# Performance work log

Hardware: AMD Instinct MI355X
Metric: run time of the kernel (lower is better)

Reference implementation:

```python
import jax, jax.numpy as jnp
import numpy as np

B = 65536
A_CH, S_CH, D_CH = 64, 256, 256
IN_CH = A_CH + S_CH + D_CH   # 576
MID = 32
OUT_CH = 4 * S_CH            # 1024
R_IN = IN_CH + S_CH          # 832

def _xavier(key, fan_in, fan_out):
    lim = np.sqrt(6.0 / (fan_in + fan_out)).astype(np.float32)
    return jax.random.uniform(key, (fan_in, fan_out), jnp.float32, -lim, lim)

def setup_inputs() -> dict:
    key = jax.random.key(0)
    ks = jax.random.split(key, 8)
    return {
        "prev_h": jax.random.normal(ks[0], (B, S_CH), jnp.float32),
        "prev_c": jax.random.normal(ks[1], (B, S_CH), jnp.float32),
        "action": jax.random.normal(ks[2], (B, A_CH), jnp.float32),
        "dynamics": jax.random.normal(ks[3], (B, D_CH), jnp.float32),
        "W1": _xavier(ks[4], IN_CH, MID),
        "b1": jnp.zeros((MID,), jnp.float32),
        "W2": _xavier(ks[5], MID, OUT_CH),
        "b2": jnp.zeros((OUT_CH,), jnp.float32),
        "Wr": _xavier(ks[6], R_IN, 1),
        "br": jnp.zeros((1,), jnp.float32),
    }

def reference(prev_h, prev_c, action, dynamics, W1, b1, W2, b2, Wr, br):
    # concat order matches torch: [dynamics, action, prev_h] -> [B, 576]
    x = jnp.concatenate([dynamics, action, prev_h], axis=1)
    h1 = jnp.tanh(x @ W1 + b1)            # fc1: tanh activation, [B, 32]
    g = h1 @ W2 + b2                       # fc2: no activation, [B, 4*S]
    act_i, act_f, hat_c, act_o = jnp.split(g, 4, axis=1)
    act_i = jax.nn.sigmoid(act_i)
    act_f = jax.nn.sigmoid(act_f)
    hat_c = jnp.tanh(hat_c)
    act_o = jax.nn.sigmoid(act_o)
    next_c = act_f * prev_c + act_i * hat_c
    next_h = act_o * jnp.tanh(next_c)
    xr = jnp.concatenate([x, next_h], axis=1)  # [B, 832]
    reward = jnp.tanh(xr @ Wr + br)            # [B, 1]
    return next_h, next_c, reward
```

## Files before the change

kernel.cpp:

```cpp
#include <hip/hip_runtime.h>
#include <hip/hip_bf16.h>

typedef float f32x4 __attribute__((ext_vector_type(4)));
typedef short bf16x8 __attribute__((ext_vector_type(8)));
typedef float float4v __attribute__((ext_vector_type(4)));

#define H1_STRIDE 40
#define W1T_K 576
#define W2T_OFF (48 * 576)

__device__ __forceinline__ short f2bf(float f) {
  __bf16 b = (__bf16)f;
  return __builtin_bit_cast(short, b);
}
__device__ __forceinline__ float fast_sigmoid(float x) {
  return __builtin_amdgcn_rcpf(1.f + __expf(-x));
}
__device__ __forceinline__ float fast_tanh(float x) {
  float e = __expf(2.f * x);
  return 1.f - 2.f * __builtin_amdgcn_rcpf(e + 1.f);
}

__global__ __launch_bounds__(256) void prep_weights(
    const float* __restrict__ W1, const float* __restrict__ W2,
    const float* __restrict__ Wr, short* __restrict__ ws)
{
  int i = blockIdx.x * 256 + threadIdx.x;
  if (i < 48 * 576) {
    int n = i / 576;
    int k = i - n * 576;
    float v = 0.f;
    if (n < 32) v = W1[k * 32 + n];
    else if (n == 32) v = Wr[k];
    ws[i] = f2bf(v);
  } else {
    int j = i - 48 * 576;
    if (j < 32 * 1024) {
      int n = j >> 5;
      int k = j & 31;
      ws[W2T_OFF + j] = f2bf(W2[k * 1024 + n]);
    }
  }
}

__global__ __launch_bounds__(256, 4) void fclstm_main(
    const float* __restrict__ prev_h, const float* __restrict__ prev_c,
    const float* __restrict__ action, const float* __restrict__ dynamics,
    const float* __restrict__ b1, const float* __restrict__ b2,
    const float* __restrict__ Wr, const float* __restrict__ br,
    const short* __restrict__ wsw,
    float* __restrict__ out_h, float* __restrict__ out_c, float* __restrict__ out_r)
{
  __shared__ short h1T[64 * H1_STRIDE];

  const int t  = threadIdx.x;
  const int r0 = blockIdx.x * 64;

  const int wid  = t >> 6;
  const int lane = t & 63;
  const int lg   = lane >> 4;
  const int ln   = lane & 15;
  const int m0   = wid << 4;
  const int rowb = r0 + m0 + 4 * lg;

  float pcA[32];
  #pragma unroll
  for (int q = 0; q < 8; ++q) {
    #pragma unroll
    for (int r = 0; r < 4; ++r)
      pcA[q * 4 + r] = prev_c[(size_t)(rowb + r) * 256 + q * 16 + ln];
  }

  f32x4 acc0 = {0.f,0.f,0.f,0.f};
  f32x4 acc1 = {0.f,0.f,0.f,0.f};
  f32x4 acc2 = {0.f,0.f,0.f,0.f};

  const int rowA = r0 + m0 + ln;
  const int kb   = 8 * lg;
  const float* dynp = dynamics + rowA * 256 + kb;
  const float* actp = action   + rowA * 64  + kb;
  const float* hp   = prev_h   + rowA * 256 + kb;
  const short* w1f  = wsw + ln * W1T_K + kb;

  auto ldfrag = [&](const float* p) -> bf16x8 {
    float4v v0 = *(const float4v*)(p);
    float4v v1 = *(const float4v*)(p + 4);
    bf16x8 a;
    a[0] = f2bf(v0.x); a[1] = f2bf(v0.y); a[2] = f2bf(v0.z); a[3] = f2bf(v0.w);
    a[4] = f2bf(v1.x); a[5] = f2bf(v1.y); a[6] = f2bf(v1.z); a[7] = f2bf(v1.w);
    return a;
  };

  #pragma unroll
  for (int j = 0; j < 18; ++j) {
    const float* src;
    if (j < 8)       src = dynp + 32 * j;
    else if (j < 10) src = actp + 32 * j - 256;
    else             src = hp   + 32 * j - 320;
    bf16x8 a  = ldfrag(src);
    bf16x8 bA = *(const bf16x8*)(w1f + 32 * j);
    bf16x8 bB = *(const bf16x8*)(w1f + 16 * W1T_K + 32 * j);
    bf16x8 bC = *(const bf16x8*)(w1f + 32 * W1T_K + 32 * j);
    acc0 = __builtin_amdgcn_mfma_f32_16x16x32_bf16(a, bA, acc0, 0, 0, 0);
    acc1 = __builtin_amdgcn_mfma_f32_16x16x32_bf16(a, bB, acc1, 0, 0, 0);
    acc2 = __builtin_amdgcn_mfma_f32_16x16x32_bf16(a, bC, acc2, 0, 0, 0);
  }

  {
    float bc0 = b1[ln], bc1 = b1[16 + ln];
    #pragma unroll
    for (int r = 0; r < 4; ++r) {
      int row = m0 + 4 * lg + r;
      h1T[row * H1_STRIDE + ln]      = f2bf(fast_tanh(acc0[r] + bc0));
      h1T[row * H1_STRIDE + 16 + ln] = f2bf(fast_tanh(acc1[r] + bc1));
    }
  }
  asm volatile("s_waitcnt lgkmcnt(0)" ::: "memory");
  __builtin_amdgcn_sched_barrier(0);
  bf16x8 af2 = *(const bf16x8*)&h1T[(m0 + ln) * H1_STRIDE + 8 * lg];

  float pcB[32];
  #pragma unroll
  for (int q = 0; q < 8; ++q) {
    #pragma unroll
    for (int r = 0; r < 4; ++r)
      pcB[q * 4 + r] = prev_c[(size_t)(rowb + r) * 256 + (q + 8) * 16 + ln];
  }

  float racc[4] = {0.f, 0.f, 0.f, 0.f};
  const float br0 = br[0];
  const short* w2t = wsw + W2T_OFF;

  auto fc2_tile = [&](int nt, float pc0, float pc1, float pc2, float pc3) {
    const int nc_ = nt * 16 + ln;
    const short* bb = w2t + nc_ * 32 + 8 * lg;
    bf16x8 bi  = *(const bf16x8*)(bb);
    bf16x8 bf_ = *(const bf16x8*)(bb + 256 * 32);
    bf16x8 bc_ = *(const bf16x8*)(bb + 512 * 32);
    bf16x8 bo  = *(const bf16x8*)(bb + 768 * 32);
    f32x4 gi = {0.f,0.f,0.f,0.f}, gf = {0.f,0.f,0.f,0.f};
    f32x4 gc = {0.f,0.f,0.f,0.f}, go = {0.f,0.f,0.f,0.f};
    gi = __builtin_amdgcn_mfma_f32_16x16x32_bf16(af2, bi,  gi, 0, 0, 0);
    gf = __builtin_amdgcn_mfma_f32_16x16x32_bf16(af2, bf_, gf, 0, 0, 0);
    gc = __builtin_amdgcn_mfma_f32_16x16x32_bf16(af2, bc_, gc, 0, 0, 0);
    go = __builtin_amdgcn_mfma_f32_16x16x32_bf16(af2, bo,  go, 0, 0, 0);
    float b2i = b2[nc_], b2f = b2[256 + nc_], b2c = b2[512 + nc_], b2o = b2[768 + nc_];
    float wrv = Wr[576 + nc_];
    float pc_[4] = {pc0, pc1, pc2, pc3};
    #pragma unroll
    for (int r = 0; r < 4; ++r) {
      int row = rowb + r;
      float iv  = fast_sigmoid(gi[r] + b2i);
      float fv  = fast_sigmoid(gf[r] + b2f);
      float cv  = fast_tanh(gc[r] + b2c);
      float ov  = fast_sigmoid(go[r] + b2o);
      float ncv = fv * pc_[r] + iv * cv;
      float nhv = ov * fast_tanh(ncv);
      __builtin_nontemporal_store(nhv, &out_h[(size_t)row * 256 + nc_]);
      __builtin_nontemporal_store(ncv, &out_c[(size_t)row * 256 + nc_]);
      racc[r] += nhv * wrv;
    }
  };

  #pragma unroll
  for (int q = 0; q < 8; ++q)
    fc2_tile(q, pcA[q * 4 + 0], pcA[q * 4 + 1], pcA[q * 4 + 2], pcA[q * 4 + 3]);
  #pragma unroll
  for (int q = 0; q < 8; ++q)
    fc2_tile(q + 8, pcB[q * 4 + 0], pcB[q * 4 + 1], pcB[q * 4 + 2], pcB[q * 4 + 3]);

  #pragma unroll
  for (int off = 1; off < 16; off <<= 1) {
    #pragma unroll
    for (int r = 0; r < 4; ++r) racc[r] += __shfl_xor(racc[r], off, 64);
  }
  if (ln == 0) {
    #pragma unroll
    for (int r = 0; r < 4; ++r) {
      float s = acc2[r] + racc[r] + br0;
      __builtin_nontemporal_store(fast_tanh(s), &out_r[rowb + r]);
    }
  }
}

extern "C" void kernel_launch(void* const* d_in, const int* in_sizes, int n_in,
                              void* d_out, int out_size, void* d_ws, size_t ws_size,
                              hipStream_t stream) {
  const float* prev_h   = (const float*)d_in[0];
  const float* prev_c   = (const float*)d_in[1];
  const float* action   = (const float*)d_in[2];
  const float* dynamics = (const float*)d_in[3];
  const float* W1 = (const float*)d_in[4];
  const float* b1 = (const float*)d_in[5];
  const float* W2 = (const float*)d_in[6];
  const float* b2 = (const float*)d_in[7];
  const float* Wr = (const float*)d_in[8];
  const float* br = (const float*)d_in[9];
  short* wsw = (short*)d_ws;

  float* out_h = (float*)d_out;
  float* out_c = out_h + (size_t)65536 * 256;
  float* out_r = out_c + (size_t)65536 * 256;

  prep_weights<<<236, 256, 0, stream>>>(W1, W2, Wr, wsw);
  fclstm_main<<<1024, 256, 0, stream>>>(prev_h, prev_c, action, dynamics,
                                        b1, b2, Wr, br, wsw, out_h, out_c, out_r);
}
```

Before: 86.66 us.

## Transpose MFMA operands for row-per-lane layout and prefetch fc1 input loads

Swaps the MFMA A/B operands so each lane owns one batch row and four consecutive output columns. prev_c loads, bias loads and out_h/out_c stores become float4 vectors, and the reward reduction shrinks to two cross-group shuffles. It also adds a 6-deep software prefetch ring for the fc1 activation loads and moves the prev_c loads to mid-loop and post-loop positions. The aim is fewer scalar global memory transactions and better latency hiding, at the cost of more live registers.

```diff
diff --git a/kernel.cpp b/kernel.cpp
--- a/kernel.cpp
+++ b/kernel.cpp
@@ -8,10 +8,14 @@
 #define H1_STRIDE 40
 #define W1T_K 576
 #define W2T_OFF (48 * 576)
+#define PF 6
 
 __device__ __forceinline__ short f2bf(float f) {
   __bf16 b = (__bf16)f;
   return __builtin_bit_cast(short, b);
+}
+__device__ __forceinline__ uint pack2(float a, float b) {
+  return (uint)(unsigned short)f2bf(a) | ((uint)(unsigned short)f2bf(b) << 16);
 }
 __device__ __forceinline__ float fast_sigmoid(float x) {
   return __builtin_amdgcn_rcpf(1.f + __expf(-x));
@@ -61,125 +65,130 @@
   const int lg   = lane >> 4;
   const int ln   = lane & 15;
   const int m0   = wid << 4;
-  const int rowb = r0 + m0 + 4 * lg;
-
-  float pcA[32];
-  #pragma unroll
-  for (int q = 0; q < 8; ++q) {
-    #pragma unroll
-    for (int r = 0; r < 4; ++r)
-      pcA[q * 4 + r] = prev_c[(size_t)(rowb + r) * 256 + q * 16 + ln];
-  }
-
-  f32x4 acc0 = {0.f,0.f,0.f,0.f};
-  f32x4 acc1 = {0.f,0.f,0.f,0.f};
-  f32x4 acc2 = {0.f,0.f,0.f,0.f};
-
   const int rowA = r0 + m0 + ln;
+
   const int kb   = 8 * lg;
   const float* dynp = dynamics + rowA * 256 + kb;
   const float* actp = action   + rowA * 64  + kb;
   const float* hp   = prev_h   + rowA * 256 + kb;
   const short* w1f  = wsw + ln * W1T_K + kb;
-
-  auto ldfrag = [&](const float* p) -> bf16x8 {
-    float4v v0 = *(const float4v*)(p);
-    float4v v1 = *(const float4v*)(p + 4);
+  const float* pcp  = prev_c + (size_t)rowA * 256 + 4 * lg;
+
+  auto asrc = [&](int j) -> const float* {
+    return (j < 8) ? (dynp + 32 * j)
+         : (j < 10) ? (actp + 32 * j - 256)
+                    : (hp + 32 * j - 320);
+  };
+
+  f32x4 acc0 = {0.f,0.f,0.f,0.f};
+  f32x4 acc1 = {0.f,0.f,0.f,0.f};
+  f32x4 acc2 = {0.f,0.f,0.f,0.f};
+
+  float4v abuf[PF][2];
+  #pragma unroll
+  for (int j = 0; j < PF; ++j) {
+    const float* p = asrc(j);
+    abuf[j][0] = *(const float4v*)p;
+    abuf[j][1] = *(const float4v*)(p + 4);
+  }
+
+  float4v pcA[8], pcB[8];
+
+  #pragma unroll
+  for (int j = 0; j < 18; ++j) {
+    const int s = j % PF;
     bf16x8 a;
-    a[0] = f2bf(v0.x); a[1] = f2bf(v0.y); a[2] = f2bf(v0.z); a[3] = f2bf(v0.w);
-    a[4] = f2bf(v1.x); a[5] = f2bf(v1.y); a[6] = f2bf(v1.z); a[7] = f2bf(v1.w);
-    return a;
-  };
-
-  #pragma unroll
-  for (int j = 0; j < 18; ++j) {
-    const float* src;
-    if (j < 8)       src = dynp + 32 * j;
-    else if (j < 10) src = actp + 32 * j - 256;
-    else             src = hp   + 32 * j - 320;
-    bf16x8 a  = ldfrag(src);
+    {
+      float4v v0 = abuf[s][0], v1 = abuf[s][1];
+      a[0] = f2bf(v0.x); a[1] = f2bf(v0.y); a[2] = f2bf(v0.z); a[3] = f2bf(v0.w);
+      a[4] = f2bf(v1.x); a[5] = f2bf(v1.y); a[6] = f2bf(v1.z); a[7] = f2bf(v1.w);
+    }
+    if (j + PF < 18) {
+      const float* p = asrc(j + PF);
+      abuf[s][0] = *(const float4v*)p;
+      abuf[s][1] = *(const float4v*)(p + 4);
+    }
+    if (j == 8) {
+      #pragma unroll
+      for (int q = 0; q < 8; ++q) pcA[q] = *(const float4v*)(pcp + q * 16);
+    }
     bf16x8 bA = *(const bf16x8*)(w1f + 32 * j);
     bf16x8 bB = *(const bf16x8*)(w1f + 16 * W1T_K + 32 * j);
     bf16x8 bC = *(const bf16x8*)(w1f + 32 * W1T_K + 32 * j);
-    acc0 = __builtin_amdgcn_mfma_f32_16x16x32_bf16(a, bA, acc0, 0, 0, 0);
-    acc1 = __builtin_amdgcn_mfma_f32_16x16x32_bf16(a, bB, acc1, 0, 0, 0);
-    acc2 = __builtin_amdgcn_mfma_f32_16x16x32_bf16(a, bC, acc2, 0, 0, 0);
-  }
+    acc0 = __builtin_amdgcn_mfma_f32_16x16x32_bf16(bA, a, acc0, 0, 0, 0);
+    acc1 = __builtin_amdgcn_mfma_f32_16x16x32_bf16(bB, a, acc1, 0, 0, 0);
+    acc2 = __builtin_amdgcn_mfma_f32_16x16x32_bf16(bC, a, acc2, 0, 0, 0);
+  }
+
+  #pragma unroll
+  for (int q = 0; q < 8; ++q) pcB[q] = *(const float4v*)(pcp + 128 + q * 16);
 
   {
-    float bc0 = b1[ln], bc1 = b1[16 + ln];
+    float4v b1lo = *(const float4v*)&b1[4 * lg];
+    float4v b1hi = *(const float4v*)&b1[16 + 4 * lg];
+    uint2 wlo, whi;
+    wlo.x = pack2(fast_tanh(acc0[0] + b1lo.x), fast_tanh(acc0[1] + b1lo.y));
+    wlo.y = pack2(fast_tanh(acc0[2] + b1lo.z), fast_tanh(acc0[3] + b1lo.w));
+    whi.x = pack2(fast_tanh(acc1[0] + b1hi.x), fast_tanh(acc1[1] + b1hi.y));
+    whi.y = pack2(fast_tanh(acc1[2] + b1hi.z), fast_tanh(acc1[3] + b1hi.w));
+    short* hrow = &h1T[(m0 + ln) * H1_STRIDE];
+    *(uint2*)(hrow + 4 * lg)      = wlo;
+    *(uint2*)(hrow + 16 + 4 * lg) = whi;
+  }
+  asm volatile("s_waitcnt lgkmcnt(0)" ::: "memory");
+  __builtin_amdgcn_sched_barrier(0);
+  bf16x8 af2 = *(const bf16x8*)(&h1T[(m0 + ln) * H1_STRIDE] + 8 * lg);
+
+  float racc = 0.f;
+  const float br0 = br[0];
+  const short* w2t = wsw + W2T_OFF;
+  const size_t orow = (size_t)rowA * 256;
+
+  auto fc2_tile = [&](int nt, float4v pc) {
+    const int c4 = nt * 16 + 4 * lg;
+    const short* aw = w2t + (nt * 16 + ln) * 32 + 8 * lg;
+    bf16x8 wi = *(const bf16x8*)(aw);
+    bf16x8 wf = *(const bf16x8*)(aw + 256 * 32);
+    bf16x8 wc = *(const bf16x8*)(aw + 512 * 32);
+    bf16x8 wo = *(const bf16x8*)(aw + 768 * 32);
+    f32x4 gi = {0.f,0.f,0.f,0.f}, gf = {0.f,0.f,0.f,0.f};
+    f32x4 gc = {0.f,0.f,0.f,0.f}, go = {0.f,0.f,0.f,0.f};
+    gi = __builtin_amdgcn_mfma_f32_16x16x32_bf16(wi, af2, gi, 0, 0, 0);
+    gf = __builtin_amdgcn_mfma_f32_16x16x32_bf16(wf, af2, gf, 0, 0, 0);
+    gc = __builtin_amdgcn_mfma_f32_16x16x32_bf16(wc, af2, gc, 0, 0, 0);
+    go = __builtin_amdgcn_mfma_f32_16x16x32_bf16(wo, af2, go, 0, 0, 0);
+    float4v b2i = *(const float4v*)&b2[c4];
+    float4v b2f = *(const float4v*)&b2[256 + c4];
+    float4v b2c = *(const float4v*)&b2[512 + c4];
+    float4v b2o = *(const float4v*)&b2[768 + c4];
+    float4v wrv = *(const float4v*)&Wr[576 + c4];
+    float4v nh, nc2;
     #pragma unroll
     for (int r = 0; r < 4; ++r) {
-      int row = m0 + 4 * lg + r;
-      h1T[row * H1_STRIDE + ln]      = f2bf(fast_tanh(acc0[r] + bc0));
-      h1T[row * H1_STRIDE + 16 + ln] = f2bf(fast_tanh(acc1[r] + bc1));
-    }
-  }
-  asm volatile("s_waitcnt lgkmcnt(0)" ::: "memory");
-  __builtin_amdgcn_sched_barrier(0);
-  bf16x8 af2 = *(const bf16x8*)&h1T[(m0 + ln) * H1_STRIDE + 8 * lg];
-
-  float pcB[32];
-  #pragma unroll
-  for (int q = 0; q < 8; ++q) {
-    #pragma unroll
-    for (int r = 0; r < 4; ++r)
-      pcB[q * 4 + r] = prev_c[(size_t)(rowb + r) * 256 + (q + 8) * 16 + ln];
-  }
-
-  float racc[4] = {0.f, 0.f, 0.f, 0.f};
-  const float br0 = br[0];
-  const short* w2t = wsw + W2T_OFF;
-
-  auto fc2_tile = [&](int nt, float pc0, float pc1, float pc2, float pc3) {
-    const int nc_ = nt * 16 + ln;
-    const short* bb = w2t + nc_ * 32 + 8 * lg;
-    bf16x8 bi  = *(const bf16x8*)(bb);
-    bf16x8 bf_ = *(const bf16x8*)(bb + 256 * 32);
-    bf16x8 bc_ = *(const bf16x8*)(bb + 512 * 32);
-    bf16x8 bo  = *(const bf16x8*)(bb + 768 * 32);
-    f32x4 gi = {0.f,0.f,0.f,0.f}, gf = {0.f,0.f,0.f,0.f};
-    f32x4 gc = {0.f,0.f,0.f,0.f}, go = {0.f,0.f,0.f,0.f};
-    gi = __builtin_amdgcn_mfma_f32_16x16x32_bf16(af2, bi,  gi, 0, 0, 0);
-    gf = __builtin_amdgcn_mfma_f32_16x16x32_bf16(af2, bf_, gf, 0, 0, 0);
-    gc = __builtin_amdgcn_mfma_f32_16x16x32_bf16(af2, bc_, gc, 0, 0, 0);
-    go = __builtin_amdgcn_mfma_f32_16x16x32_bf16(af2, bo,  go, 0, 0, 0);
-    float b2i = b2[nc_], b2f = b2[256 + nc_], b2c = b2[512 + nc_], b2o = b2[768 + nc_];
-    float wrv = Wr[576 + nc_];
-    float pc_[4] = {pc0, pc1, pc2, pc3};
-    #pragma unroll
-    for (int r = 0; r < 4; ++r) {
-      int row = rowb + r;
-      float iv  = fast_sigmoid(gi[r] + b2i);
-      float fv  = fast_sigmoid(gf[r] + b2f);
-      float cv  = fast_tanh(gc[r] + b2c);
-      float ov  = fast_sigmoid(go[r] + b2o);
-      float ncv = fv * pc_[r] + iv * cv;
+      float iv  = fast_sigmoid(gi[r] + b2i[r]);
+      float fv  = fast_sigmoid(gf[r] + b2f[r]);
+      float cv  = fast_tanh(gc[r] + b2c[r]);
+      float ov  = fast_sigmoid(go[r] + b2o[r]);
+      float ncv = fv * pc[r] + iv * cv;
       float nhv = ov * fast_tanh(ncv);
-      __builtin_nontemporal_store(nhv, &out_h[(size_t)row * 256 + nc_]);
-      __builtin_nontemporal_store(ncv, &out_c[(size_t)row * 256 + nc_]);
-      racc[r] += nhv * wrv;
-    }
+      nh[r]  = nhv;
+      nc2[r] = ncv;
+      racc += nhv * wrv[r];
+    }
+    __builtin_nontemporal_store(nh,  (float4v*)(out_h + orow + c4));
+    __builtin_nontemporal_store(nc2, (float4v*)(out_c + orow + c4));
   };
 
   #pragma unroll
-  for (int q = 0; q < 8; ++q)
-    fc2_tile(q, pcA[q * 4 + 0], pcA[q * 4 + 1], pcA[q * 4 + 2], pcA[q * 4 + 3]);
-  #pragma unroll
-  for (int q = 0; q < 8; ++q)
-    fc2_tile(q + 8, pcB[q * 4 + 0], pcB[q * 4 + 1], pcB[q * 4 + 2], pcB[q * 4 + 3]);
-
-  #pragma unroll
-  for (int off = 1; off < 16; off <<= 1) {
-    #pragma unroll
-    for (int r = 0; r < 4; ++r) racc[r] += __shfl_xor(racc[r], off, 64);
-  }
-  if (ln == 0) {
-    #pragma unroll
-    for (int r = 0; r < 4; ++r) {
-      float s = acc2[r] + racc[r] + br0;
-      __builtin_nontemporal_store(fast_tanh(s), &out_r[rowb + r]);
-    }
+  for (int q = 0; q < 8; ++q) fc2_tile(q, pcA[q]);
+  #pragma unroll
+  for (int q = 0; q < 8; ++q) fc2_tile(q + 8, pcB[q]);
+
+  racc += __shfl_xor(racc, 16, 64);
+  racc += __shfl_xor(racc, 32, 64);
+  if (lg == 0) {
+    float s = acc2[0] + racc + br0;
+    __builtin_nontemporal_store(fast_tanh(s), &out_r[rowA]);
   }
 }
 
```

Measured after the change: 92.11 us. 1.06x slower.
